# Kernel optimization log

Measured on AMD Instinct MI355X. Metric: run time of the kernel, lower is better.

Reference implementation:

```python
import jax, jax.numpy as jnp
import numpy as np

THRESH = 0.5
SCALE_POS = 2.0
SCALE_NEG = 40.0


def setup_inputs() -> dict:
    key = jax.random.key(0)
    k1, k2, k3, k4 = jax.random.split(key, 4)
    N, M, D, C = 8192, 8192, 256, 100
    emb_img = jax.random.normal(k1, (N, D), dtype=jnp.float32)
    emb_text = jax.random.normal(k2, (M, D), dtype=jnp.float32)
    # L2-normalize: cosine similarities in [-1,1], as the thresh/scale values assume
    emb_img = emb_img / jnp.linalg.norm(emb_img, axis=-1, keepdims=True)
    emb_text = emb_text / jnp.linalg.norm(emb_text, axis=-1, keepdims=True)
    gt_pre = jax.random.randint(k3, (N,), 0, C, dtype=jnp.int64 if jax.config.jax_enable_x64 else jnp.int32).astype(jnp.int32)
    gt_pres_map = jax.random.randint(k4, (M,), 0, C, dtype=jnp.int32)
    return {"emb_img": emb_img, "emb_text": emb_text, "gt_pre": gt_pre, "gt_pres_map": gt_pres_map}


def reference(emb_img, emb_text, gt_pre, gt_pres_map):
    # [N, M] pairwise similarity
    matrix = jnp.matmul(emb_img, emb_text.T)
    # vectorized equivalent of the nested python loop: z[i,j] = (gt_pre[i] == gt_pres_map[j])
    z = gt_pre[:, None] == gt_pres_map[None, :]
    # matrix_p = z*matrix; kept entries are where z==1 AND matrix>0 (same for negatives with 1-z)
    pos_mask = z & (matrix > 0)
    neg_mask = (~z) & (matrix > 0)
    pos_cnt = jnp.sum(pos_mask)
    neg_cnt = jnp.sum(neg_mask)
    pos_sum = jnp.sum(jnp.where(pos_mask, jnp.exp(-SCALE_POS * (matrix - THRESH)), 0.0))
    neg_sum = jnp.sum(jnp.where(neg_mask, jnp.exp(SCALE_NEG * (matrix - THRESH)), 0.0))
    pos_loss = jnp.where(
        pos_cnt > 0,
        jnp.log1p(pos_sum) / (SCALE_POS * jnp.maximum(pos_cnt, 1).astype(matrix.dtype)),
        jnp.zeros((), matrix.dtype),
    )
    neg_loss = jnp.where(
        neg_cnt > 0,
        jnp.log1p(neg_sum) / (SCALE_NEG * jnp.maximum(neg_cnt, 1).astype(matrix.dtype)),
        jnp.zeros((), matrix.dtype),
    )
    return pos_loss + neg_loss
```

## Files before the change

### kernel.cpp

```cpp
#include <hip/hip_runtime.h>
#include <hip/hip_bf16.h>
#include <math.h>

#define N_IMG 8192
#define M_TXT 8192
#define DIMK  256
#define BT    128
#define BK    32

typedef short bf16x8 __attribute__((ext_vector_type(8)));
typedef float f32x4  __attribute__((ext_vector_type(4)));

__device__ inline void gload_lds16(const void* g, void* l) {
    __builtin_amdgcn_global_load_lds(
        (const __attribute__((address_space(1))) unsigned int*)g,
        (__attribute__((address_space(3))) unsigned int*)l,
        16, 0, 0);
}

__device__ inline unsigned short f2bf(float x) {
    unsigned u = __float_as_uint(x);
    u += 0x7FFFu + ((u >> 16) & 1u);
    return (unsigned short)(u >> 16);
}

__global__ void convert_swz(const float* __restrict__ srcA,
                            const float* __restrict__ srcB,
                            unsigned short* __restrict__ dstA,
                            unsigned short* __restrict__ dstB,
                            double* __restrict__ accums) {
    if (blockIdx.x == 0) {
#pragma unroll
        for (int s = 0; s < 8; ++s) accums[threadIdx.x * 8 + s] = 0.0;
    }
    int q = blockIdx.x * blockDim.x + threadIdx.x;
    const int per = N_IMG * (DIMK / 8);
    const float* src; unsigned short* dst; int qq = q;
    if (q < per) { src = srcA; dst = dstA; }
    else         { src = srcB; dst = dstB; qq = q - per; }
    int r  = qq >> 5, jj = qq & 31;
    int kb = jj >> 2, j = jj & 3;
    int c  = (j - (r >> 1)) & 3;
    const float4* s = (const float4*)(src + (size_t)r * DIMK + kb * 32 + c * 8);
    float4 a = s[0], b = s[1];
    uint4 w;
    w.x = (unsigned)f2bf(a.x) | ((unsigned)f2bf(a.y) << 16);
    w.y = (unsigned)f2bf(a.z) | ((unsigned)f2bf(a.w) << 16);
    w.z = (unsigned)f2bf(b.x) | ((unsigned)f2bf(b.y) << 16);
    w.w = (unsigned)f2bf(b.z) | ((unsigned)f2bf(b.w) << 16);
    ((uint4*)dst)[qq] = w;
}

__launch_bounds__(256, 4)
__global__ void msloss_gemm(const unsigned short* __restrict__ Abf,
                            const unsigned short* __restrict__ Bbf,
                            const int* __restrict__ rowLab,
                            const int* __restrict__ colLab,
                            double* __restrict__ accums) {
    __shared__ __align__(16) unsigned short As[2][BT * BK];
    __shared__ __align__(16) unsigned short Bs[2][BT * BK];

    int tid  = threadIdx.x;
    int wave = tid >> 6, lane = tid & 63;
    int r16  = lane & 15, kg = lane >> 4;
    int wrow = (wave >> 1) * 64, wcol = (wave & 1) * 64;

    int swz = (blockIdx.x & 7) * 512 + (blockIdx.x >> 3);
    int tileRow = (swz >> 6) * BT;
    int tileCol = (swz & 63) * BT;

    int tr = tileRow + wrow, tc = tileCol + wcol;
    int4 rl4[4]; int mycl[4];
#pragma unroll
    for (int m = 0; m < 4; ++m)
        rl4[m] = *(const int4*)(rowLab + tr + m * 16 + kg * 4);
#pragma unroll
    for (int n = 0; n < 4; ++n)
        mycl[n] = colLab[tc + n * 16 + r16];

    auto STAGE = [&](int sel, int k0) {
#pragma unroll
        for (int i = 0; i < 2; ++i) {
            int p = wave * 128 + i * 64 + lane;
            int r = p >> 2, j = p & 3;
            gload_lds16(Abf + (size_t)(tileRow + r) * DIMK + k0 + j * 8,
                        &As[sel][(wave * 128 + i * 64) * 8]);
        }
#pragma unroll
        for (int i = 0; i < 2; ++i) {
            int p = wave * 128 + i * 64 + lane;
            int r = p >> 2, j = p & 3;
            gload_lds16(Bbf + (size_t)(tileCol + r) * DIMK + k0 + j * 8,
                        &Bs[sel][(wave * 128 + i * 64) * 8]);
        }
    };

    f32x4 acc[4][4] = {};

    STAGE(0, 0);

#pragma unroll 1
    for (int t = 0; t < DIMK / BK; ++t) {
        if (t < DIMK / BK - 1) {
            STAGE((t + 1) & 1, (t + 1) * BK);
            asm volatile("s_waitcnt vmcnt(4)" ::: "memory");
        } else {
            asm volatile("s_waitcnt vmcnt(0)" ::: "memory");
        }
        __builtin_amdgcn_s_barrier();
        __builtin_amdgcn_sched_barrier(0);

        const unsigned short* as = As[t & 1];
        const unsigned short* bs = Bs[t & 1];
        int slot = ((r16 >> 1) + kg) & 3;
        bf16x8 a[4], b[4];
#pragma unroll
        for (int m = 0; m < 4; ++m)
            a[m] = *(const bf16x8*)(as + (wrow + m * 16 + r16) * BK + slot * 8);
#pragma unroll
        for (int n = 0; n < 4; ++n)
            b[n] = *(const bf16x8*)(bs + (wcol + n * 16 + r16) * BK + slot * 8);
#pragma unroll
        for (int m = 0; m < 4; ++m)
#pragma unroll
            for (int n = 0; n < 4; ++n)
                acc[m][n] = __builtin_amdgcn_mfma_f32_16x16x32_bf16(
                    a[m], b[n], acc[m][n], 0, 0, 0);

        asm volatile("s_waitcnt lgkmcnt(0)" ::: "memory");
        __builtin_amdgcn_sched_barrier(0);
        __builtin_amdgcn_s_barrier();
    }

    const float CPOS = -2.8853900817779268f;
    const float CNEG = 57.707801635558536f;
    const float DPOS = 1.4426950408889634f;
    const float DNEG = -28.853900817779268f;
    const float THI  = 0.25f;

    float ps = 0.f, ns = 0.f;
    unsigned posc = 0, pec = 0;
#pragma unroll
    for (int m = 0; m < 4; ++m) {
        int lab[4] = {rl4[m].x, rl4[m].y, rl4[m].z, rl4[m].w};
#pragma unroll
        for (int j = 0; j < 4; ++j) {
            int myrl = lab[j];
#pragma unroll
            for (int n = 0; n < 4; ++n) {
                float v  = acc[m][n][j];
                bool eq  = (myrl == mycl[n]);
                bool pos = v > 0.f;
                unsigned long long bp  = __ballot(pos);
                unsigned long long bpe = bp & __ballot(eq);
                unsigned long long bhi = __ballot(v > THI);
                posc += (unsigned)__popcll(bp);
                pec  += (unsigned)__popcll(bpe);
                if (__builtin_expect((bool)(bpe | bhi), 0)) {
                    float targ = fmaf(v, eq ? CPOS : CNEG, eq ? DPOS : DNEG);
                    float e    = exp2f(pos ? targ : -100.f);
                    bool  pe   = pos && eq;
                    ps += pe ? e : 0.f;
                    ns += pe ? 0.f : e;
                }
            }
        }
    }
#pragma unroll
    for (int off = 32; off > 0; off >>= 1) {
        ps += __shfl_down(ps, off, 64);
        ns += __shfl_down(ns, off, 64);
    }
    if (lane == 0) {
        double* s = accums + ((((unsigned)blockIdx.x << 2) | (unsigned)wave) & 255u) * 8;
        atomicAdd(s + 0, (double)ps);
        atomicAdd(s + 1, (double)ns);
        atomicAdd((unsigned long long*)(s + 2), (unsigned long long)pec);
        atomicAdd((unsigned long long*)(s + 3), (unsigned long long)(posc - pec));
    }
}

__global__ void finalize_loss(const double* __restrict__ accums,
                              float* __restrict__ out) {
    int lane = threadIdx.x;
    double ps = 0, ns = 0, pc = 0, nc = 0;
#pragma unroll
    for (int s = lane; s < 256; s += 64) {
        ps += accums[s * 8 + 0];
        ns += accums[s * 8 + 1];
        pc += (double)((const unsigned long long*)accums)[s * 8 + 2];
        nc += (double)((const unsigned long long*)accums)[s * 8 + 3];
    }
#pragma unroll
    for (int off = 32; off > 0; off >>= 1) {
        ps += __shfl_down(ps, off, 64);
        ns += __shfl_down(ns, off, 64);
        pc += __shfl_down(pc, off, 64);
        nc += __shfl_down(nc, off, 64);
    }
    if (lane == 0) {
        double pl = (pc > 0.0) ? log1p(ps) / (2.0 * pc)  : 0.0;
        double nl = (nc > 0.0) ? log1p(ns) / (40.0 * nc) : 0.0;
        out[0] = (float)(pl + nl);
    }
}

extern "C" void kernel_launch(void* const* d_in, const int* in_sizes, int n_in,
                              void* d_out, int out_size, void* d_ws, size_t ws_size,
                              hipStream_t stream) {
    (void)in_sizes; (void)n_in; (void)out_size;
    const float* img    = (const float*)d_in[0];
    const float* txt    = (const float*)d_in[1];
    const int*   gt_pre = (const int*)d_in[2];
    const int*   gt_map = (const int*)d_in[3];
    float* out = (float*)d_out;

    const size_t ACC_BYTES = 256 * 8 * sizeof(double);
    const size_t MAT_BYTES = (size_t)N_IMG * DIMK * 2;
    if (ws_size < ACC_BYTES + 2 * MAT_BYTES) return;

    double*         accums = (double*)d_ws;
    unsigned short* Abf = (unsigned short*)((char*)d_ws + ACC_BYTES);
    unsigned short* Bbf = (unsigned short*)((char*)d_ws + ACC_BYTES + MAT_BYTES);

    int nchunks = 2 * N_IMG * (DIMK / 8);
    convert_swz<<<nchunks / 256, 256, 0, stream>>>(img, txt, Abf, Bbf, accums);
    msloss_gemm<<<(N_IMG / BT) * (M_TXT / BT), 256, 0, stream>>>(Abf, Bbf, gt_pre, gt_map, accums);
    finalize_loss<<<1, 64, 0, stream>>>(accums, out);
}
```

Baseline: 75.58 us.

## Chain four row tiles per block and prefetch the next tile during the epilogue

Each GEMM block now handles four 128x128 output tiles in sequence down the row dimension, so the grid is a quarter of its former size. During the last K step of each tile the block issues the first A/B stage and the row labels for the next tile, so those loads overlap the compare/exp epilogue and the atomics. The occupancy hint in the launch bounds drops from 4 to 3 blocks per CU, which gives the larger live state more registers but allows fewer resident waves. With only 1024 blocks, load balance and latency hiding across CUs may get worse, and B is re-streamed for every chained tile.

```diff
diff --git a/kernel.cpp b/kernel.cpp
--- a/kernel.cpp
+++ b/kernel.cpp
@@ -7,6 +7,7 @@
 #define DIMK  256
 #define BT    128
 #define BK    32
+#define CHAIN 4
 
 typedef short bf16x8 __attribute__((ext_vector_type(8)));
 typedef float f32x4  __attribute__((ext_vector_type(4)));
@@ -51,7 +52,7 @@
     ((uint4*)dst)[qq] = w;
 }
 
-__launch_bounds__(256, 4)
+__launch_bounds__(256, 3)
 __global__ void msloss_gemm(const unsigned short* __restrict__ Abf,
                             const unsigned short* __restrict__ Bbf,
                             const int* __restrict__ rowLab,
@@ -65,25 +66,27 @@
     int r16  = lane & 15, kg = lane >> 4;
     int wrow = (wave >> 1) * 64, wcol = (wave & 1) * 64;
 
-    int swz = (blockIdx.x & 7) * 512 + (blockIdx.x >> 3);
-    int tileRow = (swz >> 6) * BT;
-    int tileCol = (swz & 63) * BT;
-
-    int tr = tileRow + wrow, tc = tileCol + wcol;
-    int4 rl4[4]; int mycl[4];
-#pragma unroll
-    for (int m = 0; m < 4; ++m)
-        rl4[m] = *(const int4*)(rowLab + tr + m * 16 + kg * 4);
+    int bid  = blockIdx.x;
+    int swz0 = (bid & 7) * 512 + (bid >> 3);
+    int tileCol = (swz0 & 63) * BT;
+    int tileRow = (swz0 >> 6) * BT;
+    int tc = tileCol + wcol;
+
+    int mycl[4];
 #pragma unroll
     for (int n = 0; n < 4; ++n)
         mycl[n] = colLab[tc + n * 16 + r16];
-
-    auto STAGE = [&](int sel, int k0) {
+    int4 rl4[4];
+#pragma unroll
+    for (int m = 0; m < 4; ++m)
+        rl4[m] = *(const int4*)(rowLab + tileRow + wrow + m * 16 + kg * 4);
+
+    auto STAGE = [&](int sel, int k0, int trow) {
 #pragma unroll
         for (int i = 0; i < 2; ++i) {
             int p = wave * 128 + i * 64 + lane;
             int r = p >> 2, j = p & 3;
-            gload_lds16(Abf + (size_t)(tileRow + r) * DIMK + k0 + j * 8,
+            gload_lds16(Abf + (size_t)(trow + r) * DIMK + k0 + j * 8,
                         &As[sel][(wave * 128 + i * 64) * 8]);
         }
 #pragma unroll
@@ -95,88 +98,106 @@
         }
     };
 
-    f32x4 acc[4][4] = {};
-
-    STAGE(0, 0);
-
-#pragma unroll 1
-    for (int t = 0; t < DIMK / BK; ++t) {
-        if (t < DIMK / BK - 1) {
-            STAGE((t + 1) & 1, (t + 1) * BK);
-            asm volatile("s_waitcnt vmcnt(4)" ::: "memory");
-        } else {
-            asm volatile("s_waitcnt vmcnt(0)" ::: "memory");
-        }
-        __builtin_amdgcn_s_barrier();
-        __builtin_amdgcn_sched_barrier(0);
-
-        const unsigned short* as = As[t & 1];
-        const unsigned short* bs = Bs[t & 1];
-        int slot = ((r16 >> 1) + kg) & 3;
-        bf16x8 a[4], b[4];
-#pragma unroll
-        for (int m = 0; m < 4; ++m)
-            a[m] = *(const bf16x8*)(as + (wrow + m * 16 + r16) * BK + slot * 8);
-#pragma unroll
-        for (int n = 0; n < 4; ++n)
-            b[n] = *(const bf16x8*)(bs + (wcol + n * 16 + r16) * BK + slot * 8);
-#pragma unroll
-        for (int m = 0; m < 4; ++m)
-#pragma unroll
-            for (int n = 0; n < 4; ++n)
-                acc[m][n] = __builtin_amdgcn_mfma_f32_16x16x32_bf16(
-                    a[m], b[n], acc[m][n], 0, 0, 0);
-
-        asm volatile("s_waitcnt lgkmcnt(0)" ::: "memory");
-        __builtin_amdgcn_sched_barrier(0);
-        __builtin_amdgcn_s_barrier();
-    }
-
     const float CPOS = -2.8853900817779268f;
     const float CNEG = 57.707801635558536f;
     const float DPOS = 1.4426950408889634f;
     const float DNEG = -28.853900817779268f;
     const float THI  = 0.25f;
 
-    float ps = 0.f, ns = 0.f;
-    unsigned posc = 0, pec = 0;
-#pragma unroll
-    for (int m = 0; m < 4; ++m) {
-        int lab[4] = {rl4[m].x, rl4[m].y, rl4[m].z, rl4[m].w};
-#pragma unroll
-        for (int j = 0; j < 4; ++j) {
-            int myrl = lab[j];
-#pragma unroll
-            for (int n = 0; n < 4; ++n) {
-                float v  = acc[m][n][j];
-                bool eq  = (myrl == mycl[n]);
-                bool pos = v > 0.f;
-                unsigned long long bp  = __ballot(pos);
-                unsigned long long bpe = bp & __ballot(eq);
-                unsigned long long bhi = __ballot(v > THI);
-                posc += (unsigned)__popcll(bp);
-                pec  += (unsigned)__popcll(bpe);
-                if (__builtin_expect((bool)(bpe | bhi), 0)) {
-                    float targ = fmaf(v, eq ? CPOS : CNEG, eq ? DPOS : DNEG);
-                    float e    = exp2f(pos ? targ : -100.f);
-                    bool  pe   = pos && eq;
-                    ps += pe ? e : 0.f;
-                    ns += pe ? 0.f : e;
+    STAGE(0, 0, tileRow);
+
+#pragma unroll 1
+    for (int g = 0; g < CHAIN; ++g) {
+        f32x4 acc[4][4] = {};
+        int4 rl4n[4];
+
+#pragma unroll 1
+        for (int t = 0; t < DIMK / BK; ++t) {
+            if (t < DIMK / BK - 1) {
+                STAGE((t + 1) & 1, (t + 1) * BK, tileRow);
+                if (t == 0 && g > 0)
+                    asm volatile("s_waitcnt vmcnt(8)" ::: "memory");
+                else
+                    asm volatile("s_waitcnt vmcnt(4)" ::: "memory");
+            } else if (g < CHAIN - 1) {
+                STAGE(0, 0, tileRow + 2 * BT);
+#pragma unroll
+                for (int m = 0; m < 4; ++m)
+                    rl4n[m] = *(const int4*)(rowLab + tileRow + 2 * BT + wrow
+                                             + m * 16 + kg * 4);
+                asm volatile("s_waitcnt vmcnt(8)" ::: "memory");
+            } else {
+                asm volatile("s_waitcnt vmcnt(0)" ::: "memory");
+            }
+            __builtin_amdgcn_s_barrier();
+            __builtin_amdgcn_sched_barrier(0);
+
+            const unsigned short* as = As[t & 1];
+            const unsigned short* bs = Bs[t & 1];
+            int slot = ((r16 >> 1) + kg) & 3;
+            bf16x8 a[4], b[4];
+#pragma unroll
+            for (int m = 0; m < 4; ++m)
+                a[m] = *(const bf16x8*)(as + (wrow + m * 16 + r16) * BK + slot * 8);
+#pragma unroll
+            for (int n = 0; n < 4; ++n)
+                b[n] = *(const bf16x8*)(bs + (wcol + n * 16 + r16) * BK + slot * 8);
+#pragma unroll
+            for (int m = 0; m < 4; ++m)
+#pragma unroll
+                for (int n = 0; n < 4; ++n)
+                    acc[m][n] = __builtin_amdgcn_mfma_f32_16x16x32_bf16(
+                        a[m], b[n], acc[m][n], 0, 0, 0);
+
+            asm volatile("s_waitcnt lgkmcnt(0)" ::: "memory");
+            __builtin_amdgcn_sched_barrier(0);
+            __builtin_amdgcn_s_barrier();
+        }
+
+        float ps = 0.f, ns = 0.f;
+        unsigned posc = 0, pec = 0;
+#pragma unroll
+        for (int m = 0; m < 4; ++m) {
+            int lab[4] = {rl4[m].x, rl4[m].y, rl4[m].z, rl4[m].w};
+#pragma unroll
+            for (int j = 0; j < 4; ++j) {
+                int myrl = lab[j];
+#pragma unroll
+                for (int n = 0; n < 4; ++n) {
+                    float v  = acc[m][n][j];
+                    bool eq  = (myrl == mycl[n]);
+                    bool pos = v > 0.f;
+                    unsigned long long bp  = __ballot(pos);
+                    unsigned long long bpe = bp & __ballot(eq);
+                    unsigned long long bhi = __ballot(v > THI);
+                    posc += (unsigned)__popcll(bp);
+                    pec  += (unsigned)__popcll(bpe);
+                    if (__builtin_expect((bool)(bpe | bhi), 0)) {
+                        float targ = fmaf(v, eq ? CPOS : CNEG, eq ? DPOS : DNEG);
+                        float e    = exp2f(pos ? targ : -100.f);
+                        bool  pe   = pos && eq;
+                        ps += pe ? e : 0.f;
+                        ns += pe ? 0.f : e;
+                    }
                 }
             }
         }
-    }
-#pragma unroll
-    for (int off = 32; off > 0; off >>= 1) {
-        ps += __shfl_down(ps, off, 64);
-        ns += __shfl_down(ns, off, 64);
-    }
-    if (lane == 0) {
-        double* s = accums + ((((unsigned)blockIdx.x << 2) | (unsigned)wave) & 255u) * 8;
-        atomicAdd(s + 0, (double)ps);
-        atomicAdd(s + 1, (double)ns);
-        atomicAdd((unsigned long long*)(s + 2), (unsigned long long)pec);
-        atomicAdd((unsigned long long*)(s + 3), (unsigned long long)(posc - pec));
+#pragma unroll
+        for (int off = 32; off > 0; off >>= 1) {
+            ps += __shfl_down(ps, off, 64);
+            ns += __shfl_down(ns, off, 64);
+        }
+        if (lane == 0) {
+            double* s = accums + ((((unsigned)bid << 2) | (unsigned)wave) & 255u) * 8;
+            atomicAdd(s + 0, (double)ps);
+            atomicAdd(s + 1, (double)ns);
+            atomicAdd((unsigned long long*)(s + 2), (unsigned long long)pec);
+            atomicAdd((unsigned long long*)(s + 3), (unsigned long long)(posc - pec));
+        }
+
+        tileRow += 2 * BT;
+#pragma unroll
+        for (int m = 0; m < 4; ++m) rl4[m] = rl4n[m];
     }
 }
 
@@ -225,6 +246,6 @@
 
     int nchunks = 2 * N_IMG * (DIMK / 8);
     convert_swz<<<nchunks / 256, 256, 0, stream>>>(img, txt, Abf, Bbf, accums);
-    msloss_gemm<<<(N_IMG / BT) * (M_TXT / BT), 256, 0, stream>>>(Abf, Bbf, gt_pre, gt_map, accums);
+    msloss_gemm<<<(N_IMG / BT) * (M_TXT / BT) / CHAIN, 256, 0, stream>>>(Abf, Bbf, gt_pre, gt_map, accums);
     finalize_loss<<<1, 64, 0, stream>>>(accums, out);
 }
```

Result: slower. 100.1 us (+32.5%).

## Enlarge GEMM tile to 256x256 with 8 waves and triple-buffered LDS

Applied to the files above, without the earlier changes.

Block tile grows from 128x128 to 256x256 with 512 threads, so each wave computes a 128x64 sub-tile (8x4 MFMA accumulators) and gets more reuse per LDS load. LDS staging moves from double to triple buffering, which removes the trailing wait and barrier from each K iteration. The block swizzle and accumulator slot indexing are updated for the smaller grid. The cost is a doubled accumulator footprint under a 512-thread launch bound, which risks register pressure or spills, and fewer blocks in the grid.

```diff
diff --git a/kernel.cpp b/kernel.cpp
--- a/kernel.cpp
+++ b/kernel.cpp
@@ -5,7 +5,8 @@
 #define N_IMG 8192
 #define M_TXT 8192
 #define DIMK  256
-#define BT    128
+#define BTM   256
+#define BTN   256
 #define BK    32
 
 typedef short bf16x8 __attribute__((ext_vector_type(8)));
@@ -51,28 +52,29 @@
     ((uint4*)dst)[qq] = w;
 }
 
-__launch_bounds__(256, 4)
+__launch_bounds__(512, 2)
 __global__ void msloss_gemm(const unsigned short* __restrict__ Abf,
                             const unsigned short* __restrict__ Bbf,
                             const int* __restrict__ rowLab,
                             const int* __restrict__ colLab,
                             double* __restrict__ accums) {
-    __shared__ __align__(16) unsigned short As[2][BT * BK];
-    __shared__ __align__(16) unsigned short Bs[2][BT * BK];
+    __shared__ __align__(16) unsigned short As[3][BTM * BK];
+    __shared__ __align__(16) unsigned short Bs[3][BTN * BK];
 
     int tid  = threadIdx.x;
     int wave = tid >> 6, lane = tid & 63;
     int r16  = lane & 15, kg = lane >> 4;
-    int wrow = (wave >> 1) * 64, wcol = (wave & 1) * 64;
-
-    int swz = (blockIdx.x & 7) * 512 + (blockIdx.x >> 3);
-    int tileRow = (swz >> 6) * BT;
-    int tileCol = (swz & 63) * BT;
+    int wrow = (wave >> 2) * 128, wcol = (wave & 3) * 64;
+
+    int bid = blockIdx.x;
+    int swz = (bid & 7) * 128 + (bid >> 3);
+    int tileRow = (swz >> 5) * BTM;
+    int tileCol = (swz & 31) * BTN;
 
     int tr = tileRow + wrow, tc = tileCol + wcol;
-    int4 rl4[4]; int mycl[4];
-#pragma unroll
-    for (int m = 0; m < 4; ++m)
+    int4 rl4[8]; int mycl[4];
+#pragma unroll
+    for (int m = 0; m < 8; ++m)
         rl4[m] = *(const int4*)(rowLab + tr + m * 16 + kg * 4);
 #pragma unroll
     for (int n = 0; n < 4; ++n)
@@ -95,14 +97,17 @@
         }
     };
 
-    f32x4 acc[4][4] = {};
+    f32x4 acc[8][4] = {};
+    int slot = ((r16 >> 1) + kg) & 3;
 
     STAGE(0, 0);
 
+    int cur = 0;
 #pragma unroll 1
     for (int t = 0; t < DIMK / BK; ++t) {
+        int nxt = (cur == 2) ? 0 : cur + 1;
         if (t < DIMK / BK - 1) {
-            STAGE((t + 1) & 1, (t + 1) * BK);
+            STAGE(nxt, (t + 1) * BK);
             asm volatile("s_waitcnt vmcnt(4)" ::: "memory");
         } else {
             asm volatile("s_waitcnt vmcnt(0)" ::: "memory");
@@ -110,26 +115,22 @@
         __builtin_amdgcn_s_barrier();
         __builtin_amdgcn_sched_barrier(0);
 
-        const unsigned short* as = As[t & 1];
-        const unsigned short* bs = Bs[t & 1];
-        int slot = ((r16 >> 1) + kg) & 3;
-        bf16x8 a[4], b[4];
-#pragma unroll
-        for (int m = 0; m < 4; ++m)
+        const unsigned short* as = As[cur];
+        const unsigned short* bs = Bs[cur];
+        bf16x8 a[8], b[4];
+#pragma unroll
+        for (int m = 0; m < 8; ++m)
             a[m] = *(const bf16x8*)(as + (wrow + m * 16 + r16) * BK + slot * 8);
 #pragma unroll
         for (int n = 0; n < 4; ++n)
             b[n] = *(const bf16x8*)(bs + (wcol + n * 16 + r16) * BK + slot * 8);
 #pragma unroll
-        for (int m = 0; m < 4; ++m)
+        for (int m = 0; m < 8; ++m)
 #pragma unroll
             for (int n = 0; n < 4; ++n)
                 acc[m][n] = __builtin_amdgcn_mfma_f32_16x16x32_bf16(
                     a[m], b[n], acc[m][n], 0, 0, 0);
-
-        asm volatile("s_waitcnt lgkmcnt(0)" ::: "memory");
-        __builtin_amdgcn_sched_barrier(0);
-        __builtin_amdgcn_s_barrier();
+        cur = nxt;
     }
 
     const float CPOS = -2.8853900817779268f;
@@ -141,7 +142,7 @@
     float ps = 0.f, ns = 0.f;
     unsigned posc = 0, pec = 0;
 #pragma unroll
-    for (int m = 0; m < 4; ++m) {
+    for (int m = 0; m < 8; ++m) {
         int lab[4] = {rl4[m].x, rl4[m].y, rl4[m].z, rl4[m].w};
 #pragma unroll
         for (int j = 0; j < 4; ++j) {
@@ -172,7 +173,7 @@
         ns += __shfl_down(ns, off, 64);
     }
     if (lane == 0) {
-        double* s = accums + ((((unsigned)blockIdx.x << 2) | (unsigned)wave) & 255u) * 8;
+        double* s = accums + ((((unsigned)bid << 3) | (unsigned)wave) & 255u) * 8;
         atomicAdd(s + 0, (double)ps);
         atomicAdd(s + 1, (double)ns);
         atomicAdd((unsigned long long*)(s + 2), (unsigned long long)pec);
@@ -225,6 +226,6 @@
 
     int nchunks = 2 * N_IMG * (DIMK / 8);
     convert_swz<<<nchunks / 256, 256, 0, stream>>>(img, txt, Abf, Bbf, accums);
-    msloss_gemm<<<(N_IMG / BT) * (M_TXT / BT), 256, 0, stream>>>(Abf, Bbf, gt_pre, gt_map, accums);
+    msloss_gemm<<<(N_IMG / BTM) * (M_TXT / BTN), 512, 0, stream>>>(Abf, Bbf, gt_pre, gt_map, accums);
     finalize_loss<<<1, 64, 0, stream>>>(accums, out);
 }
```

Measured after the change: 101.1 us. 33.8% more time.

## Stage full K panels into LDS up front with staged vmcnt waits

Applied to the files above, without the earlier changes.

Replaces the double-buffered BK=32 K-loop with one pass that issues all eight K-slices of A and B into LDS (128 KB total) at the start. Compute then waits progressively on vmcnt counters, one quarter of the loads at a time, and drops the per-iteration trailing barriers. The aim is to keep more memory traffic in flight and cut synchronisation. In exchange, the large LDS footprint limits occupancy to one block per CU and removes overlap between blocks.

```diff
diff --git a/kernel.cpp b/kernel.cpp
--- a/kernel.cpp
+++ b/kernel.cpp
@@ -6,7 +6,6 @@
 #define M_TXT 8192
 #define DIMK  256
 #define BT    128
-#define BK    32
 
 typedef short bf16x8 __attribute__((ext_vector_type(8)));
 typedef float f32x4  __attribute__((ext_vector_type(4)));
@@ -51,21 +50,22 @@
     ((uint4*)dst)[qq] = w;
 }
 
-__launch_bounds__(256, 4)
+__launch_bounds__(256, 1)
 __global__ void msloss_gemm(const unsigned short* __restrict__ Abf,
                             const unsigned short* __restrict__ Bbf,
                             const int* __restrict__ rowLab,
                             const int* __restrict__ colLab,
                             double* __restrict__ accums) {
-    __shared__ __align__(16) unsigned short As[2][BT * BK];
-    __shared__ __align__(16) unsigned short Bs[2][BT * BK];
+    __shared__ __align__(16) unsigned short As[8][BT * 32];
+    __shared__ __align__(16) unsigned short Bs[8][BT * 32];
 
     int tid  = threadIdx.x;
     int wave = tid >> 6, lane = tid & 63;
     int r16  = lane & 15, kg = lane >> 4;
     int wrow = (wave >> 1) * 64, wcol = (wave & 1) * 64;
 
-    int swz = (blockIdx.x & 7) * 512 + (blockIdx.x >> 3);
+    int bid = blockIdx.x;
+    int swz = (bid & 7) * 512 + (bid >> 3);
     int tileRow = (swz >> 6) * BT;
     int tileCol = (swz & 63) * BT;
 
@@ -78,58 +78,56 @@
     for (int n = 0; n < 4; ++n)
         mycl[n] = colLab[tc + n * 16 + r16];
 
-    auto STAGE = [&](int sel, int k0) {
+    auto STAGE_PANEL = [&](unsigned short* panel, const unsigned short* srcM,
+                           int base, int kb) {
 #pragma unroll
         for (int i = 0; i < 2; ++i) {
-            int p = wave * 128 + i * 64 + lane;
+            int p = i * 256 + wave * 64 + lane;
             int r = p >> 2, j = p & 3;
-            gload_lds16(Abf + (size_t)(tileRow + r) * DIMK + k0 + j * 8,
-                        &As[sel][(wave * 128 + i * 64) * 8]);
-        }
-#pragma unroll
-        for (int i = 0; i < 2; ++i) {
-            int p = wave * 128 + i * 64 + lane;
-            int r = p >> 2, j = p & 3;
-            gload_lds16(Bbf + (size_t)(tileCol + r) * DIMK + k0 + j * 8,
-                        &Bs[sel][(wave * 128 + i * 64) * 8]);
+            gload_lds16(srcM + (size_t)(base + r) * DIMK + kb * 32 + j * 8,
+                        panel + (i * 256 + wave * 64) * 8);
         }
     };
 
+#pragma unroll
+    for (int s = 0; s < 4; ++s) {
+        STAGE_PANEL(As[2 * s],     Abf, tileRow, 2 * s);
+        STAGE_PANEL(As[2 * s + 1], Abf, tileRow, 2 * s + 1);
+        STAGE_PANEL(Bs[2 * s],     Bbf, tileCol, 2 * s);
+        STAGE_PANEL(Bs[2 * s + 1], Bbf, tileCol, 2 * s + 1);
+    }
+
     f32x4 acc[4][4] = {};
-
-    STAGE(0, 0);
-
-#pragma unroll 1
-    for (int t = 0; t < DIMK / BK; ++t) {
-        if (t < DIMK / BK - 1) {
-            STAGE((t + 1) & 1, (t + 1) * BK);
-            asm volatile("s_waitcnt vmcnt(4)" ::: "memory");
-        } else {
-            asm volatile("s_waitcnt vmcnt(0)" ::: "memory");
-        }
+    int slot = ((r16 >> 1) + kg) & 3;
+
+#pragma unroll
+    for (int s = 0; s < 4; ++s) {
+        if (s == 0)      asm volatile("s_waitcnt vmcnt(24)" ::: "memory");
+        else if (s == 1) asm volatile("s_waitcnt vmcnt(16)" ::: "memory");
+        else if (s == 2) asm volatile("s_waitcnt vmcnt(8)"  ::: "memory");
+        else             asm volatile("s_waitcnt vmcnt(0)"  ::: "memory");
         __builtin_amdgcn_s_barrier();
         __builtin_amdgcn_sched_barrier(0);
 
-        const unsigned short* as = As[t & 1];
-        const unsigned short* bs = Bs[t & 1];
-        int slot = ((r16 >> 1) + kg) & 3;
-        bf16x8 a[4], b[4];
-#pragma unroll
-        for (int m = 0; m < 4; ++m)
-            a[m] = *(const bf16x8*)(as + (wrow + m * 16 + r16) * BK + slot * 8);
-#pragma unroll
-        for (int n = 0; n < 4; ++n)
-            b[n] = *(const bf16x8*)(bs + (wcol + n * 16 + r16) * BK + slot * 8);
-#pragma unroll
-        for (int m = 0; m < 4; ++m)
+#pragma unroll
+        for (int th = 0; th < 2; ++th) {
+            int t = 2 * s + th;
+            const unsigned short* as = As[t];
+            const unsigned short* bs = Bs[t];
+            bf16x8 a[4], b[4];
+#pragma unroll
+            for (int m = 0; m < 4; ++m)
+                a[m] = *(const bf16x8*)(as + (wrow + m * 16 + r16) * 32 + slot * 8);
 #pragma unroll
             for (int n = 0; n < 4; ++n)
-                acc[m][n] = __builtin_amdgcn_mfma_f32_16x16x32_bf16(
-                    a[m], b[n], acc[m][n], 0, 0, 0);
-
-        asm volatile("s_waitcnt lgkmcnt(0)" ::: "memory");
-        __builtin_amdgcn_sched_barrier(0);
-        __builtin_amdgcn_s_barrier();
+                b[n] = *(const bf16x8*)(bs + (wcol + n * 16 + r16) * 32 + slot * 8);
+#pragma unroll
+            for (int m = 0; m < 4; ++m)
+#pragma unroll
+                for (int n = 0; n < 4; ++n)
+                    acc[m][n] = __builtin_amdgcn_mfma_f32_16x16x32_bf16(
+                        a[m], b[n], acc[m][n], 0, 0, 0);
+        }
     }
 
     const float CPOS = -2.8853900817779268f;
@@ -172,7 +170,7 @@
         ns += __shfl_down(ns, off, 64);
     }
     if (lane == 0) {
-        double* s = accums + ((((unsigned)blockIdx.x << 2) | (unsigned)wave) & 255u) * 8;
+        double* s = accums + ((((unsigned)bid << 2) | (unsigned)wave) & 255u) * 8;
         atomicAdd(s + 0, (double)ps);
         atomicAdd(s + 1, (double)ns);
         atomicAdd((unsigned long long*)(s + 2), (unsigned long long)pec);
```

After: 161.6 us. 114% more time.
